# Performance work log

Measured on AMD Instinct MI355X. Metric: run time of the kernel, lower is better.

Reference implementation:

```python
import jax, jax.numpy as jnp
import numpy as np

# Fixed production-scale dims (equal-size graphs -> no ragged padding needed)
B, NPG, C, H, L, FFN, NC = 16, 512, 128, 8, 4, 512, 4
D = C // H          # head dim = 16
T = NPG + 1         # +1 virtual graph token
EPG = 8192          # edges per graph (avg degree 16)
E = B * EPG


def _ln(x, g, b, eps=1e-5):
    m = x.mean(-1, keepdims=True)
    v = ((x - m) ** 2).mean(-1, keepdims=True)
    return (x - m) * jax.lax.rsqrt(v + eps) * g + b


def setup_inputs() -> dict:
    key = jax.random.key(0)
    ks = jax.random.split(key, 24)
    N = B * NPG
    node_feats = jax.random.normal(ks[0], (N, 3), jnp.float32)
    # intra-graph edges: local endpoints + per-graph node offset (matches batch_ptr math)
    local = jax.random.randint(ks[1], (2, B, EPG), 0, NPG)
    offs = (jnp.arange(B) * NPG)[None, :, None]
    edge_index = (local + offs).reshape(2, E)
    edge_attr = jax.random.randint(ks[2], (E,), 0, 10)

    def nrm(k, shape, scale=0.02):
        return jax.random.normal(k, shape, jnp.float32) * scale

    params = {
        "W_node": nrm(ks[3], (3, C), 0.3), "b_node": jnp.zeros((C,), jnp.float32),
        "graph_token": nrm(ks[4], (C,), 1.0),
        "edge_bias_table": nrm(ks[5], (11, H), 0.1).at[0].set(0.0),  # padding_idx=0
        "in_deg_emb": nrm(ks[6], (512, C)).at[0].set(0.0),           # padding_idx=0
        "out_deg_emb": nrm(ks[7], (512, C)).at[0].set(0.0),
        "vnode_bias": nrm(ks[8], (H,), 1.0),
        "Wq": nrm(ks[9], (L, C, C)), "bq": jnp.zeros((L, C), jnp.float32),
        "Wk": nrm(ks[10], (L, C, C)), "bk": jnp.zeros((L, C), jnp.float32),
        "Wv": nrm(ks[11], (L, C, C)), "bv": jnp.zeros((L, C), jnp.float32),
        "Wo": nrm(ks[12], (L, C, C)), "bo": jnp.zeros((L, C), jnp.float32),
        "ln1_g": jnp.ones((L, C), jnp.float32), "ln1_b": jnp.zeros((L, C), jnp.float32),
        "ln2_g": jnp.ones((L, C), jnp.float32), "ln2_b": jnp.zeros((L, C), jnp.float32),
        "W1": nrm(ks[13], (L, C, FFN)), "b1": jnp.zeros((L, FFN), jnp.float32),
        "W2": nrm(ks[14], (L, FFN, C)), "b2": jnp.zeros((L, C), jnp.float32),
        "normf_g": jnp.ones((C,), jnp.float32), "normf_b": jnp.zeros((C,), jnp.float32),
        "Wc1": nrm(ks[15], (C, C // 2)), "bc1": jnp.zeros((C // 2,), jnp.float32),
        "Wc2": nrm(ks[16], (C // 2, NC)), "bc2": jnp.zeros((NC,), jnp.float32),
    }
    return {"node_feats": node_feats, "edge_index": edge_index,
            "edge_attr": edge_attr, "num_graphs": B, **params}


def reference(node_feats, W_node, b_node, graph_token, edge_bias_table,
              in_deg_emb, out_deg_emb, vnode_bias,
              Wq, bq, Wk, bk, Wv, bv, Wo, bo,
              ln1_g, ln1_b, ln2_g, ln2_b, W1, b1, W2, b2,
              normf_g, normf_b, Wc1, bc1, Wc2, bc2,
              edge_index, edge_attr, num_graphs):
    N = node_feats.shape[0]
    npg = N // num_graphs
    t = npg + 1
    src, dst = edge_index[0], edge_index[1]
    # degree encoders (scatter_add of ones == segment_sum)
    in_deg = jnp.clip(jax.ops.segment_sum(jnp.ones_like(dst), dst, num_segments=N), 0, 511)
    out_deg = jnp.clip(jax.ops.segment_sum(jnp.ones_like(src), src, num_segments=N), 0, 511)
    x_enc = node_feats @ W_node + b_node + in_deg_emb[in_deg] + out_deg_emb[out_deg]
    # equal-size graphs with sorted batch ids -> padding loop is a reshape, mask all-False
    x = jnp.concatenate(
        [jnp.broadcast_to(graph_token, (num_graphs, 1, C)),
         x_enc.reshape(num_graphs, npg, C)], axis=1)  # [B, T, C]
    # attention bias: vnode row/col + scattered edge-attr embeddings
    bias = jnp.zeros((num_graphs, H, t, t), jnp.float32)
    bias = bias.at[:, :, 0, :].set(vnode_bias[None, :, None])
    bias = bias.at[:, :, :, 0].set(vnode_bias[None, :, None])
    eb = edge_bias_table[jnp.clip(edge_attr, 0, 9) + 1]  # [E, H]
    g = src // npg
    sl = src - g * npg + 1
    dl = dst - g * npg + 1
    bias = bias.at[g, :, sl, dl].add(eb)  # duplicate edges accumulate (scatter_add)
    scale = 1.0 / np.sqrt(D).astype(np.float32)
    for l in range(L):  # key_padding_mask is all-False here -> masked_fill is a no-op
        h = _ln(x, ln1_g[l], ln1_b[l])
        q = (h @ Wq[l] + bq[l]).reshape(num_graphs, t, H, D)
        k = (h @ Wk[l] + bk[l]).reshape(num_graphs, t, H, D)
        v = (h @ Wv[l] + bv[l]).reshape(num_graphs, t, H, D)
        scores = jnp.einsum('bthd,bshd->bhts', q, k) * scale + bias
        attn = jax.nn.softmax(scores, axis=-1)
        o = jnp.einsum('bhts,bshd->bthd', attn, v).reshape(num_graphs, t, C)
        x = x + o @ Wo[l] + bo[l]
        h2 = _ln(x, ln2_g[l], ln2_b[l])
        x = x + jax.nn.gelu(h2 @ W1[l] + b1[l], approximate=False) @ W2[l] + b2[l]
    x = _ln(x, normf_g, normf_b)
    gr = x[:, 0, :]  # virtual-node readout
    return jax.nn.gelu(gr @ Wc1 + bc1, approximate=False) @ Wc2 + bc2
```

## Files before the change

kernel.cpp:

```cpp
#include <hip/hip_runtime.h>
#include <hip/hip_bf16.h>

#define BB 16
#define NPG 512
#define CC 128
#define HH 8
#define LL 4
#define FFN 512
#define NCLS 4
#define DD 16
#define TT 513
#define EE 131072
#define NNODES 8192
#define ROWS (BB * TT)
#define ECAP 64
#define SP 544
#define BSTR 292

static constexpr size_t XROWS = (size_t)BB * TT;
static constexpr size_t XSZ   = XROWS * CC;
static constexpr size_t VTSZ  = (size_t)BB * HH * DD * SP;

typedef unsigned short ushort_t;
typedef __attribute__((ext_vector_type(8))) short short8;
typedef __attribute__((ext_vector_type(4))) float floatx4;

__device__ __forceinline__ float gelu_exact(float v) {
    return 0.5f * v * (1.0f + erff(v * 0.70710678118654752440f));
}
__device__ __forceinline__ ushort_t f2bf(float f) {
    union { float f; unsigned u; } c; c.f = f;
    unsigned u = c.u;
    return (ushort_t)((u + 0x7FFFu + ((u >> 16) & 1u)) >> 16);
}
__device__ __forceinline__ int swz(int row, int col, int stride) {
    int kb = col >> 3;
    return row * stride + (((kb ^ (row & 7)) << 3) | (col & 7));
}

__device__ __forceinline__ void qkv_stage4(const ushort_t* hs,
                                           const ushort_t* Wtq, const float* bq_,
                                           const ushort_t* Wtk, const float* bk_,
                                           const ushort_t* Wtv, const float* bv_,
                                           ushort_t* qb, ushort_t* kb, ushort_t* vt,
                                           int b, int t0, int wave, int lq, int quad) {
    const short* hsS = (const short*)hs;
    int n0 = wave * 32;
    int c0 = n0 + lq, c1 = n0 + 16 + lq;
    const short* Ws[3] = {(const short*)Wtq, (const short*)Wtk, (const short*)Wtv};
    const float* bs[3] = {bq_, bk_, bv_};
    size_t rB0 = (size_t)(n0 + lq) * CC, rB1 = (size_t)(n0 + 16 + lq) * CC;

    #pragma unroll
    for (int m = 0; m < 3; ++m) {
        const short* W = Ws[m];
        floatx4 a0 = {0.f,0.f,0.f,0.f}, a1 = a0;
        #pragma unroll
        for (int k0 = 0; k0 < CC; k0 += 32) {
            short8 af = *(const short8*)(hsS + swz(lq, k0 + quad * 8, 128));
            short8 b0 = *(const short8*)(W + rB0 + k0 + quad * 8);
            short8 b1 = *(const short8*)(W + rB1 + k0 + quad * 8);
            a0 = __builtin_amdgcn_mfma_f32_16x16x32_bf16(af, b0, a0, 0, 0, 0);
            a1 = __builtin_amdgcn_mfma_f32_16x16x32_bf16(af, b1, a1, 0, 0, 0);
        }
        float bv0 = bs[m][c0], bv1 = bs[m][c1];
        #pragma unroll
        for (int rg = 0; rg < 4; ++rg) {
            int t = t0 + quad * 4 + rg;
            if (t >= TT) continue;
            size_t r = (size_t)b * TT + t;
            float v0 = a0[rg] + bv0;
            float v1 = a1[rg] + bv1;
            if (m == 0) {
                qb[r * CC + c0] = f2bf(v0 * 0.25f);
                qb[r * CC + c1] = f2bf(v1 * 0.25f);
            } else if (m == 1) {
                kb[r * CC + c0] = f2bf(v0);
                kb[r * CC + c1] = f2bf(v1);
            } else {
                vt[((size_t)(b * HH + (c0 >> 4)) * DD + (c0 & 15)) * SP + t] = f2bf(v0);
                vt[((size_t)(b * HH + (c1 >> 4)) * DD + (c1 & 15)) * SP + t] = f2bf(v1);
            }
        }
    }
}

__global__ __launch_bounds__(256) void deg_csr_tr_kernel(const int* __restrict__ ei,
                                                         const int* __restrict__ ea,
                                                         int* __restrict__ deg_in,
                                                         int* __restrict__ deg_out,
                                                         int* __restrict__ cnt,
                                                         int* __restrict__ ebuf,
                                                         const float* __restrict__ Wq,
                                                         const float* __restrict__ Wk,
                                                         const float* __restrict__ Wv,
                                                         const float* __restrict__ Wo,
                                                         const float* __restrict__ W1,
                                                         const float* __restrict__ W2,
                                                         ushort_t* __restrict__ wtqkvo,
                                                         ushort_t* __restrict__ wt1,
                                                         ushort_t* __restrict__ wt2) {
    int bid = blockIdx.x;
    int tid = threadIdx.x;
    if (bid < 512) {
        int e = bid * 256 + tid;
        int src = ei[e], dst = ei[EE + e];
        atomicAdd(&deg_out[src], 1);
        atomicAdd(&deg_in[dst], 1);
        int g = src >> 9;
        int sl = src - (g << 9) + 1;
        int dl = dst - (g << 9) + 1;
        int a = ea[e];
        a = (a < 0) ? 0 : (a > 9 ? 9 : a);
        a += 1;
        int row = g * TT + sl;
        int pos = atomicAdd(&cnt[row], 1);
        if (pos < ECAP) ebuf[(size_t)row * ECAP + pos] = dl | (a << 16);
        return;
    }
    int z = bid - 512;
    const float* src; ushort_t* dst; int K, N, tile;
    if (z < 64) {
        int zz = z >> 2; tile = z & 3;
        int k = zz >> 2, l = zz & 3;
        const float* s4[4] = {Wq, Wk, Wv, Wo};
        src = s4[k] + (size_t)l * CC * CC;
        dst = wtqkvo + (size_t)(k * 4 + l) * 16384;
        K = CC; N = CC;
    } else if (z < 128) {
        int l = (z - 64) >> 4; tile = (z - 64) & 15;
        src = W1 + (size_t)l * CC * FFN;
        dst = wt1 + (size_t)l * 65536;
        K = CC; N = FFN;
    } else {
        int l = (z - 128) >> 4; tile = (z - 128) & 15;
        src = W2 + (size_t)l * FFN * CC;
        dst = wt2 + (size_t)l * 65536;
        K = FFN; N = CC;
    }
    int tilesN = N >> 6;
    int k0 = (tile / tilesN) << 6;
    int n0 = (tile - (tile / tilesN) * tilesN) << 6;
    __shared__ float t[64][65];
    int c = tid & 63, rb = tid >> 6;
    #pragma unroll
    for (int kk = 0; kk < 64; kk += 4)
        t[kk + rb][c] = src[(size_t)(k0 + kk + rb) * N + n0 + c];
    __syncthreads();
    #pragma unroll
    for (int nn = 0; nn < 64; nn += 4)
        dst[(size_t)(n0 + nn + rb) * K + k0 + c] = f2bf(t[c][nn + rb]);
}

__global__ __launch_bounds__(256) void encode_pre_kernel(const float* __restrict__ nf,
                                                         const float* __restrict__ Wn,
                                                         const float* __restrict__ bn,
                                                         const float* __restrict__ gt,
                                                         const float* __restrict__ ide,
                                                         const float* __restrict__ ode,
                                                         const int* __restrict__ deg_in,
                                                         const int* __restrict__ deg_out,
                                                         const float* __restrict__ ln1g_,
                                                         const float* __restrict__ ln1b_,
                                                         const ushort_t* __restrict__ wtqkvo,
                                                         const float* __restrict__ bq_,
                                                         const float* __restrict__ bk_,
                                                         const float* __restrict__ bv_,
                                                         float* __restrict__ x_,
                                                         ushort_t* __restrict__ qb,
                                                         ushort_t* __restrict__ kb,
                                                         ushort_t* __restrict__ vt) {
    int qt = blockIdx.x, b = blockIdx.y;
    int t0 = qt * 16;
    int tid = threadIdx.x;
    int wave = tid >> 6, lane = tid & 63, lq = lane & 15, quad = lane >> 4;

    __shared__ ushort_t hs[16 * 128];
    __shared__ float sred[4][16][2];

    int n0 = wave * 32;
    int c0 = n0 + lq, c1 = n0 + 16 + lq;
    float w0[4], w1[4];
    #pragma unroll
    for (int rg = 0; rg < 4; ++rg) {
        int t = t0 + quad * 4 + rg;
        int tc = min(t, TT - 1);
        float v0, v1;
        if (tc == 0) {
            v0 = gt[c0]; v1 = gt[c1];
        } else {
            int i = b * NPG + tc - 1;
            float f0 = nf[i*3+0], f1 = nf[i*3+1], f2 = nf[i*3+2];
            v0 = bn[c0] + f0*Wn[0*CC + c0] + f1*Wn[1*CC + c0] + f2*Wn[2*CC + c0];
            v1 = bn[c1] + f0*Wn[0*CC + c1] + f1*Wn[1*CC + c1] + f2*Wn[2*CC + c1];
            int di = min(deg_in[i], 511);
            int dq = min(deg_out[i], 511);
            v0 += ide[(size_t)di * CC + c0] + ode[(size_t)dq * CC + c0];
            v1 += ide[(size_t)di * CC + c1] + ode[(size_t)dq * CC + c1];
        }
        if (t < TT) {
            size_t r = (size_t)b * TT + t;
            x_[r * CC + c0] = v0;
            x_[r * CC + c1] = v1;
        }
        w0[rg] = v0; w1[rg] = v1;
    }
    #pragma unroll
    for (int rg = 0; rg < 4; ++rg) {
        float s1 = w0[rg] + w1[rg];
        float s2 = w0[rg]*w0[rg] + w1[rg]*w1[rg];
        #pragma unroll
        for (int m = 1; m < 16; m <<= 1) {
            s1 += __shfl_xor(s1, m, 64);
            s2 += __shfl_xor(s2, m, 64);
        }
        if (lq == 0) { sred[wave][quad*4+rg][0] = s1; sred[wave][quad*4+rg][1] = s2; }
    }
    __syncthreads();
    float g0 = ln1g_[c0], g1 = ln1g_[c1], lb0 = ln1b_[c0], lb1 = ln1b_[c1];
    #pragma unroll
    for (int rg = 0; rg < 4; ++rg) {
        int row = quad * 4 + rg;
        float S1 = sred[0][row][0] + sred[1][row][0] + sred[2][row][0] + sred[3][row][0];
        float S2 = sred[0][row][1] + sred[1][row][1] + sred[2][row][1] + sred[3][row][1];
        float mn = S1 * (1.0f/CC);
        float var = S2 * (1.0f/CC) - mn * mn;
        float rs = rsqrtf(var + 1e-5f);
        hs[swz(row, c0, 128)] = f2bf((w0[rg] - mn) * rs * g0 + lb0);
        hs[swz(row, c1, 128)] = f2bf((w1[rg] - mn) * rs * g1 + lb1);
    }
    __syncthreads();
    qkv_stage4(hs, wtqkvo, bq_,
               wtqkvo + (size_t)4 * 16384, bk_,
               wtqkvo + (size_t)8 * 16384, bv_,
               qb, kb, vt, b, t0, wave, lq, quad);
}

__global__ __launch_bounds__(256) void layer_kernel(const ushort_t* __restrict__ qbr,
                                                    const ushort_t* __restrict__ kbr,
                                                    const ushort_t* __restrict__ vtr,
                                                    const int* __restrict__ cnt,
                                                    const int* __restrict__ ebuf,
                                                    const float* __restrict__ ebt,
                                                    const float* __restrict__ vnode,
                                                    const ushort_t* __restrict__ WtO,
                                                    const float* __restrict__ bo_,
                                                    const float* __restrict__ ln2g_,
                                                    const float* __restrict__ ln2b_,
                                                    const ushort_t* __restrict__ Wt1_,
                                                    const float* __restrict__ b1_,
                                                    const ushort_t* __restrict__ Wt2_,
                                                    const float* __restrict__ b2_,
                                                    const float* __restrict__ ln1g_,
                                                    const float* __restrict__ ln1b_,
                                                    const ushort_t* __restrict__ Wtq,
                                                    const float* __restrict__ bq_,
                                                    const ushort_t* __restrict__ Wtk,
                                                    const float* __restrict__ bk_,
                                                    const ushort_t* __restrict__ Wtv,
                                                    const float* __restrict__ bv_,
                                                    const float* __restrict__ nfg,
                                                    const float* __restrict__ nfb,
                                                    const float* __restrict__ Wc1,
                                                    const float* __restrict__ bc1,
                                                    const float* __restrict__ Wc2,
                                                    const float* __restrict__ bc2,
                                                    float* __restrict__ x_,
                                                    ushort_t* __restrict__ qbw,
                                                    ushort_t* __restrict__ kbw,
                                                    ushort_t* __restrict__ vtw,
                                                    float* __restrict__ out,
                                                    int doQKV) {
    int qt = blockIdx.x, b = blockIdx.y;
    int tid = threadIdx.x;
    int wave = tid >> 6, lane = tid & 63, lq = lane & 15, quad = lane >> 4;

    __shared__ __align__(16) char smem[20480];
    float* bstrip = (float*)smem;
    ushort_t* hs = (ushort_t*)smem;
    ushort_t* ms = (ushort_t*)(smem + 4096);
    __shared__ __align__(16) ushort_t obs[16 * 128];
    __shared__ float sred[4][16][2];

    int ql = tid >> 4, e0 = tid & 15;
    int qs = qt * 16 + ql;
    int crow = b * TT + (qs < TT ? qs : 0);
    int cn = (qs > 0 && qs < TT) ? min(cnt[crow], ECAP) : 0;
    int eh[4];
    #pragma unroll
    for (int jj = 0; jj < 4; ++jj) {
        int j = e0 + jj * 16;
        eh[jj] = (j < cn) ? ebuf[(size_t)crow * ECAP + j] : -1;
    }

    int qg = qt * 16 + lq;
    int qr = qg < TT ? qg : TT - 1;
    const short* kbS = (const short*)kbr;

    for (int h = 0; h < HH; ++h) {
        __syncthreads();
        short8 qf = {0,0,0,0,0,0,0,0};
        if (quad < 2)
            qf = *(const short8*)(qbr + ((size_t)(b * TT + qr)) * CC + h * DD + quad * 8);
        float vbh = vnode[h];
        const short* vtS = (const short*)(vtr + (size_t)(b * HH + h) * DD * SP);

        floatx4 oacc = {0.f, 0.f, 0.f, 0.f};
        float lsum = 0.f;

        #pragma unroll
        for (int ch = 0; ch < 2; ++ch) {
            int sp_lo = ch ? 9 : 0;
            int sp_hi = ch ? 17 : 9;
            int s_lo  = ch ? 288 : 0;
            int nrows = ch ? 256 : 288;

            int sp = sp_lo + wave;
            short8 af0 = {0,0,0,0,0,0,0,0}, af1 = af0, vf = af0;
            if (sp < sp_hi) {
                int st0 = sp * 2, st1 = sp * 2 + 1;
                int kr0 = min(b * TT + st0 * 16 + lq, (int)XROWS - 1);
                int kr1 = min(b * TT + st1 * 16 + lq, (int)XROWS - 1);
                if (quad < 2) {
                    af0 = *(const short8*)(kbS + (size_t)kr0 * CC + h * DD + quad * 8);
                    af1 = *(const short8*)(kbS + (size_t)kr1 * CC + h * DD + quad * 8);
                }
                vf = *(const short8*)(vtS + (size_t)lq * SP + sp * 32 + quad * 8);
            }

            for (int i = tid; i < 16 * BSTR / 4; i += 256)
                ((float4*)bstrip)[i] = make_float4(0.f, 0.f, 0.f, 0.f);
            __syncthreads();
            if (ch == 0 && tid < 16) {
                int q = qt * 16 + tid;
                if (q > 0 && q < TT) bstrip[tid * BSTR] = vbh;
            }
            #pragma unroll
            for (int jj = 0; jj < 4; ++jj) {
                int e = eh[jj];
                if (e >= 0) {
                    int dl = e & 0xFFFF, a = e >> 16;
                    int loc = dl - s_lo;
                    if (loc >= 0 && loc < nrows)
                        atomicAdd(&bstrip[ql * BSTR + loc], ebt[a * 8 + h]);
                }
            }
            __syncthreads();

            for (; sp < sp_hi; sp += 4) {
                int spn = sp + 4;
                short8 nf0 = {0,0,0,0,0,0,0,0}, nf1 = nf0, nvf = nf0;
                if (spn < sp_hi) {
                    int st0 = spn * 2, st1 = spn * 2 + 1;
                    int kr0 = min(b * TT + st0 * 16 + lq, (int)XROWS - 1);
                    int kr1 = min(b * TT + st1 * 16 + lq, (int)XROWS - 1);
                    if (quad < 2) {
                        nf0 = *(const short8*)(kbS + (size_t)kr0 * CC + h * DD + quad * 8);
                        nf1 = *(const short8*)(kbS + (size_t)kr1 * CC + h * DD + quad * 8);
                    }
                    nvf = *(const short8*)(vtS + (size_t)lq * SP + spn * 32 + quad * 8);
                }

                unsigned pw[2][2];
                #pragma unroll
                for (int t = 0; t < 2; ++t) {
                    int st = sp * 2 + t;
                    floatx4 c = __builtin_amdgcn_mfma_f32_16x16x32_bf16(
                        t ? af1 : af0, qf, (floatx4){0.f, 0.f, 0.f, 0.f}, 0, 0, 0);
                    float4 bi = *(const float4*)(bstrip + lq * BSTR + (st * 16 - s_lo) + quad * 4);
                    float biv[4] = {bi.x, bi.y, bi.z, bi.w};
                    float pr[4];
                    #pragma unroll
                    for (int rg = 0; rg < 4; ++rg) {
                        int s = st * 16 + quad * 4 + rg;
                        float p = 0.f;
                        if (s < TT) p = __expf(c[rg] + biv[rg]);
                        lsum += p;
                        pr[rg] = p;
                    }
                    pw[t][0] = (unsigned)f2bf(pr[0]) | ((unsigned)f2bf(pr[1]) << 16);
                    pw[t][1] = (unsigned)f2bf(pr[2]) | ((unsigned)f2bf(pr[3]) << 16);
                }
                int srcA = lq + (((2 * quad) & 3) << 4);
                int srcB = lq + (((2 * quad + 1) & 3) << 4);
                int a00 = __shfl((int)pw[0][0], srcA, 64);
                int a01 = __shfl((int)pw[0][1], srcA, 64);
                int a10 = __shfl((int)pw[1][0], srcA, 64);
                int a11 = __shfl((int)pw[1][1], srcA, 64);
                int b00 = __shfl((int)pw[0][0], srcB, 64);
                int b01 = __shfl((int)pw[0][1], srcB, 64);
                int b10 = __shfl((int)pw[1][0], srcB, 64);
                int b11 = __shfl((int)pw[1][1], srcB, 64);
                union { int u[4]; short8 s8; } pu;
                bool lo = quad < 2;
                pu.u[0] = lo ? a00 : a10;
                pu.u[1] = lo ? a01 : a11;
                pu.u[2] = lo ? b00 : b10;
                pu.u[3] = lo ? b01 : b11;
                oacc = __builtin_amdgcn_mfma_f32_16x16x32_bf16(vf, pu.s8, oacc, 0, 0, 0);

                af0 = nf0; af1 = nf1; vf = nvf;
            }
            __syncthreads();
        }

        lsum += __shfl_xor(lsum, 16, 64);
        lsum += __shfl_xor(lsum, 32, 64);
        float* redw = (float*)smem;
        float* lsumS = (float*)smem + 1088;
        #pragma unroll
        for (int rg = 0; rg < 4; ++rg)
            redw[wave * 272 + (quad * 4 + rg) * 17 + lq] = oacc[rg];
        if (quad == 0) lsumS[wave * 16 + lq] = lsum;
        __syncthreads();
        {
            int q = tid >> 4, d = tid & 15;
            float o = 0.f, L = 0.f;
            #pragma unroll
            for (int w = 0; w < 4; ++w) {
                o += redw[w * 272 + d * 17 + q];
                L += lsumS[w * 16 + q];
            }
            obs[swz(q, h * DD + d, 128)] = f2bf(o / L);
        }
    }
    __syncthreads();

    int t0 = qt * 16;
    int n0 = wave * 32;
    int c0 = n0 + lq, c1 = n0 + 16 + lq;
    float vv0[4], vv1[4];
    const short* obsS = (const short*)obs;

    {
        const short* W = (const short*)WtO;
        size_t rB0 = (size_t)(n0 + lq) * CC, rB1 = (size_t)(n0 + 16 + lq) * CC;
        floatx4 a0 = {0.f,0.f,0.f,0.f}, a1 = a0;
        #pragma unroll
        for (int k0 = 0; k0 < CC; k0 += 32) {
            short8 af = *(const short8*)(obsS + swz(lq, k0 + quad * 8, 128));
            short8 b0 = *(const short8*)(W + rB0 + k0 + quad * 8);
            short8 b1 = *(const short8*)(W + rB1 + k0 + quad * 8);
            a0 = __builtin_amdgcn_mfma_f32_16x16x32_bf16(af, b0, a0, 0, 0, 0);
            a1 = __builtin_amdgcn_mfma_f32_16x16x32_bf16(af, b1, a1, 0, 0, 0);
        }
        float bv0 = bo_[c0], bv1 = bo_[c1];
        #pragma unroll
        for (int rg = 0; rg < 4; ++rg) {
            int t = t0 + quad * 4 + rg;
            size_t rc = (size_t)b * TT + min(t, TT - 1);
            vv0[rg] = a0[rg] + bv0 + x_[rc * CC + c0];
            vv1[rg] = a1[rg] + bv1 + x_[rc * CC + c1];
        }
        #pragma unroll
        for (int rg = 0; rg < 4; ++rg) {
            float s1 = vv0[rg] + vv1[rg];
            float s2 = vv0[rg]*vv0[rg] + vv1[rg]*vv1[rg];
            #pragma unroll
            for (int m = 1; m < 16; m <<= 1) {
                s1 += __shfl_xor(s1, m, 64);
                s2 += __shfl_xor(s2, m, 64);
            }
            if (lq == 0) { sred[wave][quad*4+rg][0] = s1; sred[wave][quad*4+rg][1] = s2; }
        }
        __syncthreads();
        float g0 = ln2g_[c0], g1 = ln2g_[c1], lb0 = ln2b_[c0], lb1 = ln2b_[c1];
        #pragma unroll
        for (int rg = 0; rg < 4; ++rg) {
            int row = quad * 4 + rg;
            float S1 = sred[0][row][0] + sred[1][row][0] + sred[2][row][0] + sred[3][row][0];
            float S2 = sred[0][row][1] + sred[1][row][1] + sred[2][row][1] + sred[3][row][1];
            float mn = S1 * (1.0f/CC);
            float var = S2 * (1.0f/CC) - mn * mn;
            float rs = rsqrtf(var + 1e-5f);
            hs[swz(row, c0, 128)] = f2bf((vv0[rg] - mn) * rs * g0 + lb0);
            hs[swz(row, c1, 128)] = f2bf((vv1[rg] - mn) * rs * g1 + lb1);
        }
    }
    __syncthreads();

    {
        const short* hsS = (const short*)hs;
        const short* W = (const short*)Wt1_;
        #pragma unroll
        for (int nt = 0; nt < 4; ++nt) {
            int n = wave * 128 + nt * 32;
            size_t rB0 = (size_t)(n + lq) * CC, rB1 = (size_t)(n + 16 + lq) * CC;
            floatx4 a0 = {0.f,0.f,0.f,0.f}, a1 = a0;
            #pragma unroll
            for (int k0 = 0; k0 < CC; k0 += 32) {
                short8 af = *(const short8*)(hsS + swz(lq, k0 + quad * 8, 128));
                short8 b0 = *(const short8*)(W + rB0 + k0 + quad * 8);
                short8 b1 = *(const short8*)(W + rB1 + k0 + quad * 8);
                a0 = __builtin_amdgcn_mfma_f32_16x16x32_bf16(af, b0, a0, 0, 0, 0);
                a1 = __builtin_amdgcn_mfma_f32_16x16x32_bf16(af, b1, a1, 0, 0, 0);
            }
            float bb0 = b1_[n + lq], bb1 = b1_[n + 16 + lq];
            #pragma unroll
            for (int rg = 0; rg < 4; ++rg) {
                int row = quad * 4 + rg;
                ms[swz(row, n + lq, 512)]      = f2bf(gelu_exact(a0[rg] + bb0));
                ms[swz(row, n + 16 + lq, 512)] = f2bf(gelu_exact(a1[rg] + bb1));
            }
        }
    }
    __syncthreads();

    float w0[4], w1[4];
    {
        const short* msS = (const short*)ms;
        const short* W = (const short*)Wt2_;
        size_t rB0 = (size_t)(n0 + lq) * FFN, rB1 = (size_t)(n0 + 16 + lq) * FFN;
        floatx4 a0 = {0.f,0.f,0.f,0.f}, a1 = a0;
        #pragma unroll 8
        for (int k0 = 0; k0 < FFN; k0 += 32) {
            short8 af = *(const short8*)(msS + swz(lq, k0 + quad * 8, 512));
            short8 b0 = *(const short8*)(W + rB0 + k0 + quad * 8);
            short8 b1 = *(const short8*)(W + rB1 + k0 + quad * 8);
            a0 = __builtin_amdgcn_mfma_f32_16x16x32_bf16(af, b0, a0, 0, 0, 0);
            a1 = __builtin_amdgcn_mfma_f32_16x16x32_bf16(af, b1, a1, 0, 0, 0);
        }
        float bv0 = b2_[c0], bv1 = b2_[c1];
        #pragma unroll
        for (int rg = 0; rg < 4; ++rg) {
            int t = t0 + quad * 4 + rg;
            w0[rg] = a0[rg] + bv0 + vv0[rg];
            w1[rg] = a1[rg] + bv1 + vv1[rg];
            if (t < TT) {
                size_t r = (size_t)b * TT + t;
                x_[r * CC + c0] = w0[rg];
                x_[r * CC + c1] = w1[rg];
            }
        }
    }

    if (doQKV) {
        #pragma unroll
        for (int rg = 0; rg < 4; ++rg) {
            float s1 = w0[rg] + w1[rg];
            float s2 = w0[rg]*w0[rg] + w1[rg]*w1[rg];
            #pragma unroll
            for (int m = 1; m < 16; m <<= 1) {
                s1 += __shfl_xor(s1, m, 64);
                s2 += __shfl_xor(s2, m, 64);
            }
            if (lq == 0) { sred[wave][quad*4+rg][0] = s1; sred[wave][quad*4+rg][1] = s2; }
        }
        __syncthreads();
        float g0 = ln1g_[c0], g1 = ln1g_[c1], lb0 = ln1b_[c0], lb1 = ln1b_[c1];
        #pragma unroll
        for (int rg = 0; rg < 4; ++rg) {
            int row = quad * 4 + rg;
            float S1 = sred[0][row][0] + sred[1][row][0] + sred[2][row][0] + sred[3][row][0];
            float S2 = sred[0][row][1] + sred[1][row][1] + sred[2][row][1] + sred[3][row][1];
            float mn = S1 * (1.0f/CC);
            float var = S2 * (1.0f/CC) - mn * mn;
            float rs = rsqrtf(var + 1e-5f);
            hs[swz(row, c0, 128)] = f2bf((w0[rg] - mn) * rs * g0 + lb0);
            hs[swz(row, c1, 128)] = f2bf((w1[rg] - mn) * rs * g1 + lb1);
        }
        __syncthreads();
        qkv_stage4(hs, Wtq, bq_, Wtk, bk_, Wtv, bv_, qbw, kbw, vtw, b, t0, wave, lq, quad);
        return;
    }

    if (qt != 0) return;

    __syncthreads();
    float* hrow = (float*)ms;
    float* xfs  = hrow + CC;
    float* c1s  = xfs + CC;
    float* red  = c1s + 64;
    #pragma unroll
    for (int rg = 0; rg < 4; ++rg) {
        if (quad * 4 + rg == 0) { hrow[c0] = w0[rg]; hrow[c1] = w1[rg]; }
    }
    __syncthreads();

    {
        int c = tid;
        float v = 0.f, s1 = 0.f, s2 = 0.f;
        if (c < CC) { v = hrow[c]; s1 = v; s2 = v * v; }
        #pragma unroll
        for (int m = 32; m >= 1; m >>= 1) {
            s1 += __shfl_xor(s1, m, 64);
            s2 += __shfl_xor(s2, m, 64);
        }
        int w = c >> 6;
        if (c < CC && (c & 63) == 0) { red[w*2] = s1; red[w*2+1] = s2; }
        __syncthreads();
        if (c < CC) {
            float S1 = red[0] + red[2], S2 = red[1] + red[3];
            float mn = S1 * (1.0f/CC);
            float var = S2 * (1.0f/CC) - mn * mn;
            float rs = rsqrtf(var + 1e-5f);
            xfs[c] = (v - mn) * rs * nfg[c] + nfb[c];
        }
        __syncthreads();
        if (c < 64) {
            float acc = bc1[c];
            #pragma unroll 4
            for (int k = 0; k < CC; ++k) acc = fmaf(xfs[k], Wc1[(size_t)k * 64 + c], acc);
            c1s[c] = gelu_exact(acc);
        }
        __syncthreads();
        if (c < NCLS) {
            float acc = bc2[c];
            #pragma unroll 4
            for (int j = 0; j < 64; ++j) acc = fmaf(c1s[j], Wc2[(size_t)j * NCLS + c], acc);
            out[(size_t)b * NCLS + c] = acc;
        }
    }
}

extern "C" void kernel_launch(void* const* d_in, const int* in_sizes, int n_in,
                              void* d_out, int out_size, void* d_ws, size_t ws_size,
                              hipStream_t stream) {
    const float* node_feats = (const float*)d_in[0];
    const int*   edge_index = (const int*)d_in[1];
    const int*   edge_attr  = (const int*)d_in[2];
    const float* W_node  = (const float*)d_in[4];
    const float* b_node  = (const float*)d_in[5];
    const float* g_token = (const float*)d_in[6];
    const float* ebt     = (const float*)d_in[7];
    const float* ide     = (const float*)d_in[8];
    const float* ode     = (const float*)d_in[9];
    const float* vnode   = (const float*)d_in[10];
    const float* Wq = (const float*)d_in[11];
    const float* bq = (const float*)d_in[12];
    const float* Wk = (const float*)d_in[13];
    const float* bk = (const float*)d_in[14];
    const float* Wv = (const float*)d_in[15];
    const float* bv = (const float*)d_in[16];
    const float* Wo = (const float*)d_in[17];
    const float* bo = (const float*)d_in[18];
    const float* ln1g = (const float*)d_in[19];
    const float* ln1b = (const float*)d_in[20];
    const float* ln2g = (const float*)d_in[21];
    const float* ln2b = (const float*)d_in[22];
    const float* W1 = (const float*)d_in[23];
    const float* b1 = (const float*)d_in[24];
    const float* W2 = (const float*)d_in[25];
    const float* b2 = (const float*)d_in[26];
    const float* nfg = (const float*)d_in[27];
    const float* nfb = (const float*)d_in[28];
    const float* Wc1 = (const float*)d_in[29];
    const float* bc1 = (const float*)d_in[30];
    const float* Wc2 = (const float*)d_in[31];
    const float* bc2 = (const float*)d_in[32];
    float* out = (float*)d_out;

    char* base = (char*)d_ws;
    float* x      = (float*)base;     base += XSZ * 4;
    ushort_t* qb0 = (ushort_t*)base;  base += XSZ * 2;
    ushort_t* kb0 = (ushort_t*)base;  base += XSZ * 2;
    ushort_t* vt0 = (ushort_t*)base;  base += VTSZ * 2;
    ushort_t* qb1 = (ushort_t*)base;  base += XSZ * 2;
    ushort_t* kb1 = (ushort_t*)base;  base += XSZ * 2;
    ushort_t* vt1 = (ushort_t*)base;  base += VTSZ * 2;
    ushort_t* wtqkvo = (ushort_t*)base; base += (size_t)16 * 16384 * 2;
    ushort_t* wt1 = (ushort_t*)base;  base += (size_t)4 * 65536 * 2;
    ushort_t* wt2 = (ushort_t*)base;  base += (size_t)4 * 65536 * 2;
    int* deg_in  = (int*)base;        base += NNODES * 4;
    int* deg_out = (int*)base;        base += NNODES * 4;
    int* cnt     = (int*)base;        base += (size_t)ROWS * 4;
    int* ebuf    = (int*)base;        base += (size_t)ROWS * ECAP * 4;

    ushort_t* qbs[2] = {qb0, qb1};
    ushort_t* kbs[2] = {kb0, kb1};
    ushort_t* vts[2] = {vt0, vt1};

    hipMemsetAsync(deg_in, 0, (size_t)(2 * NNODES + ROWS) * 4, stream);
    deg_csr_tr_kernel<<<512 + 192, 256, 0, stream>>>(
        edge_index, edge_attr, deg_in, deg_out, cnt, ebuf,
        Wq, Wk, Wv, Wo, W1, W2, wtqkvo, wt1, wt2);

    encode_pre_kernel<<<dim3(33, BB), 256, 0, stream>>>(
        node_feats, W_node, b_node, g_token, ide, ode, deg_in, deg_out,
        ln1g, ln1b, wtqkvo, bq, bk, bv, x, qb0, kb0, vt0);

    for (int l = 0; l < LL; ++l) {
        int rd = l & 1, wr = rd ^ 1;
        int ln = (l + 1) % LL;
        layer_kernel<<<dim3(33, BB), 256, 0, stream>>>(
            qbs[rd], kbs[rd], vts[rd], cnt, ebuf, ebt, vnode,
            wtqkvo + (size_t)(12 + l)*16384, bo + l*CC,
            ln2g + l*CC, ln2b + l*CC,
            wt1 + (size_t)l*65536, b1 + l*FFN,
            wt2 + (size_t)l*65536, b2 + l*CC,
            ln1g + ln*CC, ln1b + ln*CC,
            wtqkvo + (size_t)(0 + ln)*16384, bq + ln*CC,
            wtqkvo + (size_t)(4 + ln)*16384, bk + ln*CC,
            wtqkvo + (size_t)(8 + ln)*16384, bv + ln*CC,
            nfg, nfb, Wc1, bc1, Wc2, bc2,
            x, qbs[wr], kbs[wr], vts[wr], out,
            (l < LL-1) ? 1 : 0);
    }
}
```

Baseline: 474.2 us.

## Precompute dense bf16 edge-bias tensor once and widen blocks to 512 threads

Adds a pre-pass, run inside the same pre_kernel launch, that builds a dense bf16 attention-bias tensor [B,H,513,544] from the per-row edge lists. Each layer then reads this tensor instead of rebuilding the sparse bias from cnt/ebuf four times. Separately, every kernel moves from 4 to 8 waves per block, with each wave handling 16 output columns instead of 32, to raise parallelism. The cost is a roughly 36 MB extra bias buffer that must be streamed from memory in every layer, plus more synchronisation per block.

```diff
diff --git a/kernel.cpp b/kernel.cpp
--- a/kernel.cpp
+++ b/kernel.cpp
@@ -15,11 +15,12 @@
 #define ROWS (BB * TT)
 #define ECAP 64
 #define SP 544
-#define BSTR 292
+#define BPAD 544
 
 static constexpr size_t XROWS = (size_t)BB * TT;
 static constexpr size_t XSZ   = XROWS * CC;
 static constexpr size_t VTSZ  = (size_t)BB * HH * DD * SP;
+static constexpr size_t BIASSZ = (size_t)BB * HH * 513 * BPAD;
 
 typedef unsigned short ushort_t;
 typedef __attribute__((ext_vector_type(8))) short short8;
@@ -33,53 +34,49 @@
     unsigned u = c.u;
     return (ushort_t)((u + 0x7FFFu + ((u >> 16) & 1u)) >> 16);
 }
+__device__ __forceinline__ float bf2f(ushort_t u) {
+    union { unsigned u; float f; } c; c.u = ((unsigned)u) << 16; return c.f;
+}
 __device__ __forceinline__ int swz(int row, int col, int stride) {
     int kb = col >> 3;
     return row * stride + (((kb ^ (row & 7)) << 3) | (col & 7));
 }
 
-__device__ __forceinline__ void qkv_stage4(const ushort_t* hs,
+__device__ __forceinline__ void qkv_stage8(const ushort_t* hs,
                                            const ushort_t* Wtq, const float* bq_,
                                            const ushort_t* Wtk, const float* bk_,
                                            const ushort_t* Wtv, const float* bv_,
                                            ushort_t* qb, ushort_t* kb, ushort_t* vt,
                                            int b, int t0, int wave, int lq, int quad) {
     const short* hsS = (const short*)hs;
-    int n0 = wave * 32;
-    int c0 = n0 + lq, c1 = n0 + 16 + lq;
+    int c = wave * 16 + lq;
     const short* Ws[3] = {(const short*)Wtq, (const short*)Wtk, (const short*)Wtv};
     const float* bs[3] = {bq_, bk_, bv_};
-    size_t rB0 = (size_t)(n0 + lq) * CC, rB1 = (size_t)(n0 + 16 + lq) * CC;
+    size_t rB = (size_t)c * CC;
 
     #pragma unroll
     for (int m = 0; m < 3; ++m) {
         const short* W = Ws[m];
-        floatx4 a0 = {0.f,0.f,0.f,0.f}, a1 = a0;
+        floatx4 a0 = {0.f,0.f,0.f,0.f};
         #pragma unroll
         for (int k0 = 0; k0 < CC; k0 += 32) {
             short8 af = *(const short8*)(hsS + swz(lq, k0 + quad * 8, 128));
-            short8 b0 = *(const short8*)(W + rB0 + k0 + quad * 8);
-            short8 b1 = *(const short8*)(W + rB1 + k0 + quad * 8);
+            short8 b0 = *(const short8*)(W + rB + k0 + quad * 8);
             a0 = __builtin_amdgcn_mfma_f32_16x16x32_bf16(af, b0, a0, 0, 0, 0);
-            a1 = __builtin_amdgcn_mfma_f32_16x16x32_bf16(af, b1, a1, 0, 0, 0);
-        }
-        float bv0 = bs[m][c0], bv1 = bs[m][c1];
+        }
+        float bv0 = bs[m][c];
         #pragma unroll
         for (int rg = 0; rg < 4; ++rg) {
             int t = t0 + quad * 4 + rg;
             if (t >= TT) continue;
             size_t r = (size_t)b * TT + t;
             float v0 = a0[rg] + bv0;
-            float v1 = a1[rg] + bv1;
             if (m == 0) {
-                qb[r * CC + c0] = f2bf(v0 * 0.25f);
-                qb[r * CC + c1] = f2bf(v1 * 0.25f);
+                qb[r * CC + c] = f2bf(v0 * 0.25f);
             } else if (m == 1) {
-                kb[r * CC + c0] = f2bf(v0);
-                kb[r * CC + c1] = f2bf(v1);
+                kb[r * CC + c] = f2bf(v0);
             } else {
-                vt[((size_t)(b * HH + (c0 >> 4)) * DD + (c0 & 15)) * SP + t] = f2bf(v0);
-                vt[((size_t)(b * HH + (c1 >> 4)) * DD + (c1 & 15)) * SP + t] = f2bf(v1);
+                vt[((size_t)(b * HH + wave) * DD + lq) * SP + t] = f2bf(v0);
             }
         }
     }
@@ -152,63 +149,87 @@
         dst[(size_t)(n0 + nn + rb) * K + k0 + c] = f2bf(t[c][nn + rb]);
 }
 
-__global__ __launch_bounds__(256) void encode_pre_kernel(const float* __restrict__ nf,
-                                                         const float* __restrict__ Wn,
-                                                         const float* __restrict__ bn,
-                                                         const float* __restrict__ gt,
-                                                         const float* __restrict__ ide,
-                                                         const float* __restrict__ ode,
-                                                         const int* __restrict__ deg_in,
-                                                         const int* __restrict__ deg_out,
-                                                         const float* __restrict__ ln1g_,
-                                                         const float* __restrict__ ln1b_,
-                                                         const ushort_t* __restrict__ wtqkvo,
-                                                         const float* __restrict__ bq_,
-                                                         const float* __restrict__ bk_,
-                                                         const float* __restrict__ bv_,
-                                                         float* __restrict__ x_,
-                                                         ushort_t* __restrict__ qb,
-                                                         ushort_t* __restrict__ kb,
-                                                         ushort_t* __restrict__ vt) {
-    int qt = blockIdx.x, b = blockIdx.y;
+__global__ __launch_bounds__(512) void pre_kernel(const float* __restrict__ nf,
+                                                  const float* __restrict__ Wn,
+                                                  const float* __restrict__ bn,
+                                                  const float* __restrict__ gt,
+                                                  const float* __restrict__ ide,
+                                                  const float* __restrict__ ode,
+                                                  const int* __restrict__ deg_in,
+                                                  const int* __restrict__ deg_out,
+                                                  const float* __restrict__ ln1g_,
+                                                  const float* __restrict__ ln1b_,
+                                                  const ushort_t* __restrict__ wtqkvo,
+                                                  const float* __restrict__ bq_,
+                                                  const float* __restrict__ bk_,
+                                                  const float* __restrict__ bv_,
+                                                  float* __restrict__ x_,
+                                                  ushort_t* __restrict__ qb,
+                                                  ushort_t* __restrict__ kb,
+                                                  ushort_t* __restrict__ vt,
+                                                  const int* __restrict__ cnt,
+                                                  const int* __restrict__ ebuf,
+                                                  const float* __restrict__ ebt,
+                                                  ushort_t* __restrict__ bias_d) {
+    int bid = blockIdx.x;
+    int tid = threadIdx.x;
+    __shared__ __align__(16) char parena[17408];
+
+    if (bid >= 528) {
+        int z = bid - 528;
+        int b = z / 513;
+        int sl = z - b * 513;
+        float* row8 = (float*)parena;
+        for (int i = tid; i < 8 * BPAD / 4; i += 512)
+            ((float4*)row8)[i] = make_float4(0.f, 0.f, 0.f, 0.f);
+        __syncthreads();
+        int crow = b * TT + sl;
+        int cn = min(cnt[crow], ECAP);
+        int h = tid & 7;
+        for (int j = tid >> 3; j < cn; j += 64) {
+            int e = ebuf[(size_t)crow * ECAP + j];
+            atomicAdd(&row8[h * BPAD + (e & 0xFFFF)], ebt[(e >> 16) * 8 + h]);
+        }
+        __syncthreads();
+        #pragma unroll
+        for (int hh = 0; hh < HH; ++hh) {
+            size_t base = ((size_t)(b * HH + hh) * 513 + sl) * BPAD;
+            for (int s = tid; s < BPAD; s += 512)
+                bias_d[base + s] = f2bf(row8[hh * BPAD + s]);
+        }
+        return;
+    }
+
+    int b = bid / 33, qt = bid - b * 33;
     int t0 = qt * 16;
-    int tid = threadIdx.x;
     int wave = tid >> 6, lane = tid & 63, lq = lane & 15, quad = lane >> 4;
-
-    __shared__ ushort_t hs[16 * 128];
-    __shared__ float sred[4][16][2];
-
-    int n0 = wave * 32;
-    int c0 = n0 + lq, c1 = n0 + 16 + lq;
-    float w0[4], w1[4];
+    ushort_t* hs = (ushort_t*)parena;
+    auto sred = (float (*)[16][2])(parena + 4096);
+
+    int c = wave * 16 + lq;
+    float w0[4];
     #pragma unroll
     for (int rg = 0; rg < 4; ++rg) {
         int t = t0 + quad * 4 + rg;
         int tc = min(t, TT - 1);
-        float v0, v1;
+        float v0;
         if (tc == 0) {
-            v0 = gt[c0]; v1 = gt[c1];
+            v0 = gt[c];
         } else {
             int i = b * NPG + tc - 1;
             float f0 = nf[i*3+0], f1 = nf[i*3+1], f2 = nf[i*3+2];
-            v0 = bn[c0] + f0*Wn[0*CC + c0] + f1*Wn[1*CC + c0] + f2*Wn[2*CC + c0];
-            v1 = bn[c1] + f0*Wn[0*CC + c1] + f1*Wn[1*CC + c1] + f2*Wn[2*CC + c1];
+            v0 = bn[c] + f0*Wn[0*CC + c] + f1*Wn[1*CC + c] + f2*Wn[2*CC + c];
             int di = min(deg_in[i], 511);
             int dq = min(deg_out[i], 511);
-            v0 += ide[(size_t)di * CC + c0] + ode[(size_t)dq * CC + c0];
-            v1 += ide[(size_t)di * CC + c1] + ode[(size_t)dq * CC + c1];
-        }
-        if (t < TT) {
-            size_t r = (size_t)b * TT + t;
-            x_[r * CC + c0] = v0;
-            x_[r * CC + c1] = v1;
-        }
-        w0[rg] = v0; w1[rg] = v1;
+            v0 += ide[(size_t)di * CC + c] + ode[(size_t)dq * CC + c];
+        }
+        if (t < TT) x_[((size_t)b * TT + t) * CC + c] = v0;
+        w0[rg] = v0;
     }
     #pragma unroll
     for (int rg = 0; rg < 4; ++rg) {
-        float s1 = w0[rg] + w1[rg];
-        float s2 = w0[rg]*w0[rg] + w1[rg]*w1[rg];
+        float s1 = w0[rg];
+        float s2 = w0[rg] * w0[rg];
         #pragma unroll
         for (int m = 1; m < 16; m <<= 1) {
             s1 += __shfl_xor(s1, m, 64);
@@ -217,245 +238,192 @@
         if (lq == 0) { sred[wave][quad*4+rg][0] = s1; sred[wave][quad*4+rg][1] = s2; }
     }
     __syncthreads();
-    float g0 = ln1g_[c0], g1 = ln1g_[c1], lb0 = ln1b_[c0], lb1 = ln1b_[c1];
+    float g0 = ln1g_[c], lb0 = ln1b_[c];
     #pragma unroll
     for (int rg = 0; rg < 4; ++rg) {
         int row = quad * 4 + rg;
-        float S1 = sred[0][row][0] + sred[1][row][0] + sred[2][row][0] + sred[3][row][0];
-        float S2 = sred[0][row][1] + sred[1][row][1] + sred[2][row][1] + sred[3][row][1];
+        float S1 = 0.f, S2 = 0.f;
+        #pragma unroll
+        for (int w = 0; w < 8; ++w) { S1 += sred[w][row][0]; S2 += sred[w][row][1]; }
         float mn = S1 * (1.0f/CC);
         float var = S2 * (1.0f/CC) - mn * mn;
         float rs = rsqrtf(var + 1e-5f);
-        hs[swz(row, c0, 128)] = f2bf((w0[rg] - mn) * rs * g0 + lb0);
-        hs[swz(row, c1, 128)] = f2bf((w1[rg] - mn) * rs * g1 + lb1);
-    }
-    __syncthreads();
-    qkv_stage4(hs, wtqkvo, bq_,
+        hs[swz(row, c, 128)] = f2bf((w0[rg] - mn) * rs * g0 + lb0);
+    }
+    __syncthreads();
+    qkv_stage8(hs, wtqkvo, bq_,
                wtqkvo + (size_t)4 * 16384, bk_,
                wtqkvo + (size_t)8 * 16384, bv_,
                qb, kb, vt, b, t0, wave, lq, quad);
 }
 
-__global__ __launch_bounds__(256) void layer_kernel(const ushort_t* __restrict__ qbr,
-                                                    const ushort_t* __restrict__ kbr,
-                                                    const ushort_t* __restrict__ vtr,
-                                                    const int* __restrict__ cnt,
-                                                    const int* __restrict__ ebuf,
-                                                    const float* __restrict__ ebt,
-                                                    const float* __restrict__ vnode,
-                                                    const ushort_t* __restrict__ WtO,
-                                                    const float* __restrict__ bo_,
-                                                    const float* __restrict__ ln2g_,
-                                                    const float* __restrict__ ln2b_,
-                                                    const ushort_t* __restrict__ Wt1_,
-                                                    const float* __restrict__ b1_,
-                                                    const ushort_t* __restrict__ Wt2_,
-                                                    const float* __restrict__ b2_,
-                                                    const float* __restrict__ ln1g_,
-                                                    const float* __restrict__ ln1b_,
-                                                    const ushort_t* __restrict__ Wtq,
-                                                    const float* __restrict__ bq_,
-                                                    const ushort_t* __restrict__ Wtk,
-                                                    const float* __restrict__ bk_,
-                                                    const ushort_t* __restrict__ Wtv,
-                                                    const float* __restrict__ bv_,
-                                                    const float* __restrict__ nfg,
-                                                    const float* __restrict__ nfb,
-                                                    const float* __restrict__ Wc1,
-                                                    const float* __restrict__ bc1,
-                                                    const float* __restrict__ Wc2,
-                                                    const float* __restrict__ bc2,
-                                                    float* __restrict__ x_,
-                                                    ushort_t* __restrict__ qbw,
-                                                    ushort_t* __restrict__ kbw,
-                                                    ushort_t* __restrict__ vtw,
-                                                    float* __restrict__ out,
-                                                    int doQKV) {
+__global__ __launch_bounds__(512, 4) void layer_kernel(const ushort_t* __restrict__ qbr,
+                                                       const ushort_t* __restrict__ kbr,
+                                                       const ushort_t* __restrict__ vtr,
+                                                       const ushort_t* __restrict__ bias_d,
+                                                       const float* __restrict__ vnode,
+                                                       const ushort_t* __restrict__ WtO,
+                                                       const float* __restrict__ bo_,
+                                                       const float* __restrict__ ln2g_,
+                                                       const float* __restrict__ ln2b_,
+                                                       const ushort_t* __restrict__ Wt1_,
+                                                       const float* __restrict__ b1_,
+                                                       const ushort_t* __restrict__ Wt2_,
+                                                       const float* __restrict__ b2_,
+                                                       const float* __restrict__ ln1g_,
+                                                       const float* __restrict__ ln1b_,
+                                                       const ushort_t* __restrict__ Wtq,
+                                                       const float* __restrict__ bq_,
+                                                       const ushort_t* __restrict__ Wtk,
+                                                       const float* __restrict__ bk_,
+                                                       const ushort_t* __restrict__ Wtv,
+                                                       const float* __restrict__ bv_,
+                                                       const float* __restrict__ nfg,
+                                                       const float* __restrict__ nfb,
+                                                       const float* __restrict__ Wc1,
+                                                       const float* __restrict__ bc1,
+                                                       const float* __restrict__ Wc2,
+                                                       const float* __restrict__ bc2,
+                                                       float* __restrict__ x_,
+                                                       ushort_t* __restrict__ qbw,
+                                                       ushort_t* __restrict__ kbw,
+                                                       ushort_t* __restrict__ vtw,
+                                                       float* __restrict__ out,
+                                                       int doQKV) {
     int qt = blockIdx.x, b = blockIdx.y;
     int tid = threadIdx.x;
     int wave = tid >> 6, lane = tid & 63, lq = lane & 15, quad = lane >> 4;
 
     __shared__ __align__(16) char smem[20480];
-    float* bstrip = (float*)smem;
     ushort_t* hs = (ushort_t*)smem;
     ushort_t* ms = (ushort_t*)(smem + 4096);
     __shared__ __align__(16) ushort_t obs[16 * 128];
-    __shared__ float sred[4][16][2];
-
-    int ql = tid >> 4, e0 = tid & 15;
-    int qs = qt * 16 + ql;
-    int crow = b * TT + (qs < TT ? qs : 0);
-    int cn = (qs > 0 && qs < TT) ? min(cnt[crow], ECAP) : 0;
-    int eh[4];
-    #pragma unroll
-    for (int jj = 0; jj < 4; ++jj) {
-        int j = e0 + jj * 16;
-        eh[jj] = (j < cn) ? ebuf[(size_t)crow * ECAP + j] : -1;
-    }
-
-    int qg = qt * 16 + lq;
-    int qr = qg < TT ? qg : TT - 1;
-    const short* kbS = (const short*)kbr;
-
-    for (int h = 0; h < HH; ++h) {
-        __syncthreads();
-        short8 qf = {0,0,0,0,0,0,0,0};
+    __shared__ float sred[8][16][2];
+
+    {
+        int h = wave;
+        int qg = qt * 16 + lq;
+        int qr = min(qg, TT - 1);
+        short8 z8 = {0,0,0,0,0,0,0,0};
+        short8 qf = z8;
         if (quad < 2)
             qf = *(const short8*)(qbr + ((size_t)(b * TT + qr)) * CC + h * DD + quad * 8);
-        float vbh = vnode[h];
+        float vn = vnode[h];
+        const short* kbS = (const short*)kbr;
         const short* vtS = (const short*)(vtr + (size_t)(b * HH + h) * DD * SP);
+        const ushort_t* brow = bias_d + ((size_t)(b * HH + h) * 513 + qr) * BPAD;
+
+        short8 af0c = z8, af1c = z8, vfc;
+        {
+            int kr0 = min(b * TT + lq, (int)XROWS - 1);
+            int kr1 = min(b * TT + 16 + lq, (int)XROWS - 1);
+            if (quad < 2) {
+                af0c = *(const short8*)(kbS + (size_t)kr0 * CC + h * DD + quad * 8);
+                af1c = *(const short8*)(kbS + (size_t)kr1 * CC + h * DD + quad * 8);
+            }
+            vfc = *(const short8*)(vtS + (size_t)lq * SP + quad * 8);
+        }
+        uint2 bi0c = *(const uint2*)(brow + quad * 4);
+        uint2 bi1c = *(const uint2*)(brow + 16 + quad * 4);
 
         floatx4 oacc = {0.f, 0.f, 0.f, 0.f};
         float lsum = 0.f;
 
-        #pragma unroll
-        for (int ch = 0; ch < 2; ++ch) {
-            int sp_lo = ch ? 9 : 0;
-            int sp_hi = ch ? 17 : 9;
-            int s_lo  = ch ? 288 : 0;
-            int nrows = ch ? 256 : 288;
-
-            int sp = sp_lo + wave;
-            short8 af0 = {0,0,0,0,0,0,0,0}, af1 = af0, vf = af0;
-            if (sp < sp_hi) {
-                int st0 = sp * 2, st1 = sp * 2 + 1;
+        for (int sp = 0; sp < 17; ++sp) {
+            int spn = sp + 1;
+            short8 af0n = z8, af1n = z8, vfn = z8;
+            uint2 bi0n = make_uint2(0u, 0u), bi1n = make_uint2(0u, 0u);
+            if (spn < 17) {
+                int st0 = spn * 2, st1 = st0 + 1;
                 int kr0 = min(b * TT + st0 * 16 + lq, (int)XROWS - 1);
                 int kr1 = min(b * TT + st1 * 16 + lq, (int)XROWS - 1);
                 if (quad < 2) {
-                    af0 = *(const short8*)(kbS + (size_t)kr0 * CC + h * DD + quad * 8);
-                    af1 = *(const short8*)(kbS + (size_t)kr1 * CC + h * DD + quad * 8);
+                    af0n = *(const short8*)(kbS + (size_t)kr0 * CC + h * DD + quad * 8);
+                    af1n = *(const short8*)(kbS + (size_t)kr1 * CC + h * DD + quad * 8);
                 }
-                vf = *(const short8*)(vtS + (size_t)lq * SP + sp * 32 + quad * 8);
+                vfn = *(const short8*)(vtS + (size_t)lq * SP + spn * 32 + quad * 8);
+                bi0n = *(const uint2*)(brow + spn * 32 + quad * 4);
+                bi1n = *(const uint2*)(brow + spn * 32 + 16 + quad * 4);
             }
-
-            for (int i = tid; i < 16 * BSTR / 4; i += 256)
-                ((float4*)bstrip)[i] = make_float4(0.f, 0.f, 0.f, 0.f);
-            __syncthreads();
-            if (ch == 0 && tid < 16) {
-                int q = qt * 16 + tid;
-                if (q > 0 && q < TT) bstrip[tid * BSTR] = vbh;
+            float vadd = ((sp == 0) & (quad == 0) & (qg > 0)) ? vn : 0.f;
+
+            unsigned pw[2][2];
+            #pragma unroll
+            for (int t = 0; t < 2; ++t) {
+                int st = sp * 2 + t;
+                floatx4 cc4 = __builtin_amdgcn_mfma_f32_16x16x32_bf16(
+                    t ? af1c : af0c, qf, (floatx4){0.f, 0.f, 0.f, 0.f}, 0, 0, 0);
+                uint2 bi = t ? bi1c : bi0c;
+                float pr[4];
+                #pragma unroll
+                for (int rg = 0; rg < 4; ++rg) {
+                    int s = st * 16 + quad * 4 + rg;
+                    unsigned bw = (rg < 2) ? bi.x : bi.y;
+                    float bb = bf2f((rg & 1) ? (ushort_t)(bw >> 16) : (ushort_t)(bw & 0xFFFFu));
+                    if (t == 0 && rg == 0) bb += vadd;
+                    float p = 0.f;
+                    if (s < TT) p = __expf(cc4[rg] + bb);
+                    lsum += p;
+                    pr[rg] = p;
+                }
+                pw[t][0] = (unsigned)f2bf(pr[0]) | ((unsigned)f2bf(pr[1]) << 16);
+                pw[t][1] = (unsigned)f2bf(pr[2]) | ((unsigned)f2bf(pr[3]) << 16);
             }
-            #pragma unroll
-            for (int jj = 0; jj < 4; ++jj) {
-                int e = eh[jj];
-                if (e >= 0) {
-                    int dl = e & 0xFFFF, a = e >> 16;
-                    int loc = dl - s_lo;
-                    if (loc >= 0 && loc < nrows)
-                        atomicAdd(&bstrip[ql * BSTR + loc], ebt[a * 8 + h]);
-                }
-            }
-            __syncthreads();
-
-            for (; sp < sp_hi; sp += 4) {
-                int spn = sp + 4;
-                short8 nf0 = {0,0,0,0,0,0,0,0}, nf1 = nf0, nvf = nf0;
-                if (spn < sp_hi) {
-                    int st0 = spn * 2, st1 = spn * 2 + 1;
-                    int kr0 = min(b * TT + st0 * 16 + lq, (int)XROWS - 1);
-                    int kr1 = min(b * TT + st1 * 16 + lq, (int)XROWS - 1);
-                    if (quad < 2) {
-                        nf0 = *(const short8*)(kbS + (size_t)kr0 * CC + h * DD + quad * 8);
-                        nf1 = *(const short8*)(kbS + (size_t)kr1 * CC + h * DD + quad * 8);
-                    }
-                    nvf = *(const short8*)(vtS + (size_t)lq * SP + spn * 32 + quad * 8);
-                }
-
-                unsigned pw[2][2];
-                #pragma unroll
-                for (int t = 0; t < 2; ++t) {
-                    int st = sp * 2 + t;
-                    floatx4 c = __builtin_amdgcn_mfma_f32_16x16x32_bf16(
-                        t ? af1 : af0, qf, (floatx4){0.f, 0.f, 0.f, 0.f}, 0, 0, 0);
-                    float4 bi = *(const float4*)(bstrip + lq * BSTR + (st * 16 - s_lo) + quad * 4);
-                    float biv[4] = {bi.x, bi.y, bi.z, bi.w};
-                    float pr[4];
-                    #pragma unroll
-                    for (int rg = 0; rg < 4; ++rg) {
-                        int s = st * 16 + quad * 4 + rg;
-                        float p = 0.f;
-                        if (s < TT) p = __expf(c[rg] + biv[rg]);
-                        lsum += p;
-                        pr[rg] = p;
-                    }
-                    pw[t][0] = (unsigned)f2bf(pr[0]) | ((unsigned)f2bf(pr[1]) << 16);
-                    pw[t][1] = (unsigned)f2bf(pr[2]) | ((unsigned)f2bf(pr[3]) << 16);
-                }
-                int srcA = lq + (((2 * quad) & 3) << 4);
-                int srcB = lq + (((2 * quad + 1) & 3) << 4);
-                int a00 = __shfl((int)pw[0][0], srcA, 64);
-                int a01 = __shfl((int)pw[0][1], srcA, 64);
-                int a10 = __shfl((int)pw[1][0], srcA, 64);
-                int a11 = __shfl((int)pw[1][1], srcA, 64);
-                int b00 = __shfl((int)pw[0][0], srcB, 64);
-                int b01 = __shfl((int)pw[0][1], srcB, 64);
-                int b10 = __shfl((int)pw[1][0], srcB, 64);
-                int b11 = __shfl((int)pw[1][1], srcB, 64);
-                union { int u[4]; short8 s8; } pu;
-                bool lo = quad < 2;
-                pu.u[0] = lo ? a00 : a10;
-                pu.u[1] = lo ? a01 : a11;
-                pu.u[2] = lo ? b00 : b10;
-                pu.u[3] = lo ? b01 : b11;
-                oacc = __builtin_amdgcn_mfma_f32_16x16x32_bf16(vf, pu.s8, oacc, 0, 0, 0);
-
-                af0 = nf0; af1 = nf1; vf = nvf;
-            }
-            __syncthreads();
+            int srcA = lq + (((2 * quad) & 3) << 4);
+            int srcB = lq + (((2 * quad + 1) & 3) << 4);
+            int a00 = __shfl((int)pw[0][0], srcA, 64);
+            int a01 = __shfl((int)pw[0][1], srcA, 64);
+            int a10 = __shfl((int)pw[1][0], srcA, 64);
+            int a11 = __shfl((int)pw[1][1], srcA, 64);
+            int b00 = __shfl((int)pw[0][0], srcB, 64);
+            int b01 = __shfl((int)pw[0][1], srcB, 64);
+            int b10 = __shfl((int)pw[1][0], srcB, 64);
+            int b11 = __shfl((int)pw[1][1], srcB, 64);
+            union { int u[4]; short8 s8; } pu;
+            bool lo = quad < 2;
+            pu.u[0] = lo ? a00 : a10;
+            pu.u[1] = lo ? a01 : a11;
+            pu.u[2] = lo ? b00 : b10;
+            pu.u[3] = lo ? b01 : b11;
+            oacc = __builtin_amdgcn_mfma_f32_16x16x32_bf16(vfc, pu.s8, oacc, 0, 0, 0);
+
+            af0c = af0n; af1c = af1n; vfc = vfn; bi0c = bi0n; bi1c = bi1n;
         }
 
         lsum += __shfl_xor(lsum, 16, 64);
         lsum += __shfl_xor(lsum, 32, 64);
-        float* redw = (float*)smem;
-        float* lsumS = (float*)smem + 1088;
         #pragma unroll
         for (int rg = 0; rg < 4; ++rg)
-            redw[wave * 272 + (quad * 4 + rg) * 17 + lq] = oacc[rg];
-        if (quad == 0) lsumS[wave * 16 + lq] = lsum;
-        __syncthreads();
-        {
-            int q = tid >> 4, d = tid & 15;
-            float o = 0.f, L = 0.f;
-            #pragma unroll
-            for (int w = 0; w < 4; ++w) {
-                o += redw[w * 272 + d * 17 + q];
-                L += lsumS[w * 16 + q];
-            }
-            obs[swz(q, h * DD + d, 128)] = f2bf(o / L);
-        }
+            obs[swz(lq, h * DD + quad * 4 + rg, 128)] = f2bf(oacc[rg] / lsum);
     }
     __syncthreads();
 
     int t0 = qt * 16;
-    int n0 = wave * 32;
-    int c0 = n0 + lq, c1 = n0 + 16 + lq;
-    float vv0[4], vv1[4];
+    int c = wave * 16 + lq;
+    float vv0[4];
     const short* obsS = (const short*)obs;
 
     {
         const short* W = (const short*)WtO;
-        size_t rB0 = (size_t)(n0 + lq) * CC, rB1 = (size_t)(n0 + 16 + lq) * CC;
-        floatx4 a0 = {0.f,0.f,0.f,0.f}, a1 = a0;
+        size_t rB = (size_t)c * CC;
+        floatx4 a0 = {0.f,0.f,0.f,0.f};
         #pragma unroll
         for (int k0 = 0; k0 < CC; k0 += 32) {
             short8 af = *(const short8*)(obsS + swz(lq, k0 + quad * 8, 128));
-            short8 b0 = *(const short8*)(W + rB0 + k0 + quad * 8);
-            short8 b1 = *(const short8*)(W + rB1 + k0 + quad * 8);
+            short8 b0 = *(const short8*)(W + rB + k0 + quad * 8);
             a0 = __builtin_amdgcn_mfma_f32_16x16x32_bf16(af, b0, a0, 0, 0, 0);
-            a1 = __builtin_amdgcn_mfma_f32_16x16x32_bf16(af, b1, a1, 0, 0, 0);
-        }
-        float bv0 = bo_[c0], bv1 = bo_[c1];
+        }
+        float bv0 = bo_[c];
         #pragma unroll
         for (int rg = 0; rg < 4; ++rg) {
             int t = t0 + quad * 4 + rg;
             size_t rc = (size_t)b * TT + min(t, TT - 1);
-            vv0[rg] = a0[rg] + bv0 + x_[rc * CC + c0];
-            vv1[rg] = a1[rg] + bv1 + x_[rc * CC + c1];
+            vv0[rg] = a0[rg] + bv0 + x_[rc * CC + c];
         }
         #pragma unroll
         for (int rg = 0; rg < 4; ++rg) {
-            float s1 = vv0[rg] + vv1[rg];
-            float s2 = vv0[rg]*vv0[rg] + vv1[rg]*vv1[rg];
+            float s1 = vv0[rg];
+            float s2 = vv0[rg] * vv0[rg];
             #pragma unroll
             for (int m = 1; m < 16; m <<= 1) {
                 s1 += __shfl_xor(s1, m, 64);
@@ -464,17 +432,17 @@
             if (lq == 0) { sred[wave][quad*4+rg][0] = s1; sred[wave][quad*4+rg][1] = s2; }
         }
         __syncthreads();
-        float g0 = ln2g_[c0], g1 = ln2g_[c1], lb0 = ln2b_[c0], lb1 = ln2b_[c1];
+        float g0 = ln2g_[c], lb0 = ln2b_[c];
         #pragma unroll
         for (int rg = 0; rg < 4; ++rg) {
             int row = quad * 4 + rg;
-            float S1 = sred[0][row][0] + sred[1][row][0] + sred[2][row][0] + sred[3][row][0];
-            float S2 = sred[0][row][1] + sred[1][row][1] + sred[2][row][1] + sred[3][row][1];
+            float S1 = 0.f, S2 = 0.f;
+            #pragma unroll
+            for (int w = 0; w < 8; ++w) { S1 += sred[w][row][0]; S2 += sred[w][row][1]; }
             float mn = S1 * (1.0f/CC);
             float var = S2 * (1.0f/CC) - mn * mn;
             float rs = rsqrtf(var + 1e-5f);
-            hs[swz(row, c0, 128)] = f2bf((vv0[rg] - mn) * rs * g0 + lb0);
-            hs[swz(row, c1, 128)] = f2bf((vv1[rg] - mn) * rs * g1 + lb1);
+            hs[swz(row, c, 128)] = f2bf((vv0[rg] - mn) * rs * g0 + lb0);
         }
     }
     __syncthreads();
@@ -484,61 +452,49 @@
         const short* W = (const short*)Wt1_;
         #pragma unroll
         for (int nt = 0; nt < 4; ++nt) {
-            int n = wave * 128 + nt * 32;
-            size_t rB0 = (size_t)(n + lq) * CC, rB1 = (size_t)(n + 16 + lq) * CC;
-            floatx4 a0 = {0.f,0.f,0.f,0.f}, a1 = a0;
+            int n = wave * 64 + nt * 16;
+            size_t rB = (size_t)(n + lq) * CC;
+            floatx4 a0 = {0.f,0.f,0.f,0.f};
             #pragma unroll
             for (int k0 = 0; k0 < CC; k0 += 32) {
                 short8 af = *(const short8*)(hsS + swz(lq, k0 + quad * 8, 128));
-                short8 b0 = *(const short8*)(W + rB0 + k0 + quad * 8);
-                short8 b1 = *(const short8*)(W + rB1 + k0 + quad * 8);
+                short8 b0 = *(const short8*)(W + rB + k0 + quad * 8);
                 a0 = __builtin_amdgcn_mfma_f32_16x16x32_bf16(af, b0, a0, 0, 0, 0);
-                a1 = __builtin_amdgcn_mfma_f32_16x16x32_bf16(af, b1, a1, 0, 0, 0);
             }
-            float bb0 = b1_[n + lq], bb1 = b1_[n + 16 + lq];
+            float bb0 = b1_[n + lq];
             #pragma unroll
-            for (int rg = 0; rg < 4; ++rg) {
-                int row = quad * 4 + rg;
-                ms[swz(row, n + lq, 512)]      = f2bf(gelu_exact(a0[rg] + bb0));
-                ms[swz(row, n + 16 + lq, 512)] = f2bf(gelu_exact(a1[rg] + bb1));
-            }
-        }
-    }
-    __syncthreads();
-
-    float w0[4], w1[4];
+            for (int rg = 0; rg < 4; ++rg)
+                ms[swz(quad * 4 + rg, n + lq, 512)] = f2bf(gelu_exact(a0[rg] + bb0));
+        }
+    }
+    __syncthreads();
+
+    float w0[4];
     {
         const short* msS = (const short*)ms;
         const short* W = (const short*)Wt2_;
-        size_t rB0 = (size_t)(n0 + lq) * FFN, rB1 = (size_t)(n0 + 16 + lq) * FFN;
-        floatx4 a0 = {0.f,0.f,0.f,0.f}, a1 = a0;
+        size_t rB = (size_t)c * FFN;
+        floatx4 a0 = {0.f,0.f,0.f,0.f};
         #pragma unroll 8
         for (int k0 = 0; k0 < FFN; k0 += 32) {
             short8 af = *(const short8*)(msS + swz(lq, k0 + quad * 8, 512));
-            short8 b0 = *(const short8*)(W + rB0 + k0 + quad * 8);
-            short8 b1 = *(const short8*)(W + rB1 + k0 + quad * 8);
+            short8 b0 = *(const short8*)(W + rB + k0 + quad * 8);
             a0 = __builtin_amdgcn_mfma_f32_16x16x32_bf16(af, b0, a0, 0, 0, 0);
-            a1 = __builtin_amdgcn_mfma_f32_16x16x32_bf16(af, b1, a1, 0, 0, 0);
-        }
-        float bv0 = b2_[c0], bv1 = b2_[c1];
+        }
+        float bv0 = b2_[c];
         #pragma unroll
         for (int rg = 0; rg < 4; ++rg) {
             int t = t0 + quad * 4 + rg;
             w0[rg] = a0[rg] + bv0 + vv0[rg];
-            w1[rg] = a1[rg] + bv1 + vv1[rg];
-            if (t < TT) {
-                size_t r = (size_t)b * TT + t;
-                x_[r * CC + c0] = w0[rg];
-                x_[r * CC + c1] = w1[rg];
-            }
+            if (t < TT) x_[((size_t)b * TT + t) * CC + c] = w0[rg];
         }
     }
 
     if (doQKV) {
         #pragma unroll
         for (int rg = 0; rg < 4; ++rg) {
-            float s1 = w0[rg] + w1[rg];
-            float s2 = w0[rg]*w0[rg] + w1[rg]*w1[rg];
+            float s1 = w0[rg];
+            float s2 = w0[rg] * w0[rg];
             #pragma unroll
             for (int m = 1; m < 16; m <<= 1) {
                 s1 += __shfl_xor(s1, m, 64);
@@ -547,20 +503,20 @@
             if (lq == 0) { sred[wave][quad*4+rg][0] = s1; sred[wave][quad*4+rg][1] = s2; }
         }
         __syncthreads();
-        float g0 = ln1g_[c0], g1 = ln1g_[c1], lb0 = ln1b_[c0], lb1 = ln1b_[c1];
+        float g0 = ln1g_[c], lb0 = ln1b_[c];
         #pragma unroll
         for (int rg = 0; rg < 4; ++rg) {
             int row = quad * 4 + rg;
-            float S1 = sred[0][row][0] + sred[1][row][0] + sred[2][row][0] + sred[3][row][0];
-            float S2 = sred[0][row][1] + sred[1][row][1] + sred[2][row][1] + sred[3][row][1];
+            float S1 = 0.f, S2 = 0.f;
+            #pragma unroll
+            for (int w = 0; w < 8; ++w) { S1 += sred[w][row][0]; S2 += sred[w][row][1]; }
             float mn = S1 * (1.0f/CC);
             float var = S2 * (1.0f/CC) - mn * mn;
             float rs = rsqrtf(var + 1e-5f);
-            hs[swz(row, c0, 128)] = f2bf((w0[rg] - mn) * rs * g0 + lb0);
-            hs[swz(row, c1, 128)] = f2bf((w1[rg] - mn) * rs * g1 + lb1);
-        }
-        __syncthreads();
-        qkv_stage4(hs, Wtq, bq_, Wtk, bk_, Wtv, bv_, qbw, kbw, vtw, b, t0, wave, lq, quad);
+            hs[swz(row, c, 128)] = f2bf((w0[rg] - mn) * rs * g0 + lb0);
+        }
+        __syncthreads();
+        qkv_stage8(hs, Wtq, bq_, Wtk, bk_, Wtv, bv_, qbw, kbw, vtw, b, t0, wave, lq, quad);
         return;
     }
 
@@ -571,44 +527,41 @@
     float* xfs  = hrow + CC;
     float* c1s  = xfs + CC;
     float* red  = c1s + 64;
-    #pragma unroll
-    for (int rg = 0; rg < 4; ++rg) {
-        if (quad * 4 + rg == 0) { hrow[c0] = w0[rg]; hrow[c1] = w1[rg]; }
-    }
+    if (quad == 0) hrow[c] = w0[0];
     __syncthreads();
 
     {
-        int c = tid;
+        int ct = tid;
         float v = 0.f, s1 = 0.f, s2 = 0.f;
-        if (c < CC) { v = hrow[c]; s1 = v; s2 = v * v; }
+        if (ct < CC) { v = hrow[ct]; s1 = v; s2 = v * v; }
         #pragma unroll
         for (int m = 32; m >= 1; m >>= 1) {
             s1 += __shfl_xor(s1, m, 64);
             s2 += __shfl_xor(s2, m, 64);
         }
-        int w = c >> 6;
-        if (c < CC && (c & 63) == 0) { red[w*2] = s1; red[w*2+1] = s2; }
-        __syncthreads();
-        if (c < CC) {
+        int w = ct >> 6;
+        if (ct < CC && (ct & 63) == 0) { red[w*2] = s1; red[w*2+1] = s2; }
+        __syncthreads();
+        if (ct < CC) {
             float S1 = red[0] + red[2], S2 = red[1] + red[3];
             float mn = S1 * (1.0f/CC);
             float var = S2 * (1.0f/CC) - mn * mn;
             float rs = rsqrtf(var + 1e-5f);
-            xfs[c] = (v - mn) * rs * nfg[c] + nfb[c];
-        }
-        __syncthreads();
-        if (c < 64) {
-            float acc = bc1[c];
+            xfs[ct] = (v - mn) * rs * nfg[ct] + nfb[ct];
+        }
+        __syncthreads();
+        if (ct < 64) {
+            float acc = bc1[ct];
             #pragma unroll 4
-            for (int k = 0; k < CC; ++k) acc = fmaf(xfs[k], Wc1[(size_t)k * 64 + c], acc);
-            c1s[c] = gelu_exact(acc);
-        }
-        __syncthreads();
-        if (c < NCLS) {
-            float acc = bc2[c];
+            for (int k = 0; k < CC; ++k) acc = fmaf(xfs[k], Wc1[(size_t)k * 64 + ct], acc);
+            c1s[ct] = gelu_exact(acc);
+        }
+        __syncthreads();
+        if (ct < NCLS) {
+            float acc = bc2[ct];
             #pragma unroll 4
-            for (int j = 0; j < 64; ++j) acc = fmaf(c1s[j], Wc2[(size_t)j * NCLS + c], acc);
-            out[(size_t)b * NCLS + c] = acc;
+            for (int j = 0; j < 64; ++j) acc = fmaf(c1s[j], Wc2[(size_t)j * NCLS + ct], acc);
+            out[(size_t)b * NCLS + ct] = acc;
         }
     }
 }
@@ -661,6 +614,7 @@
     ushort_t* wtqkvo = (ushort_t*)base; base += (size_t)16 * 16384 * 2;
     ushort_t* wt1 = (ushort_t*)base;  base += (size_t)4 * 65536 * 2;
     ushort_t* wt2 = (ushort_t*)base;  base += (size_t)4 * 65536 * 2;
+    ushort_t* bias_d = (ushort_t*)base; base += BIASSZ * 2;
     int* deg_in  = (int*)base;        base += NNODES * 4;
     int* deg_out = (int*)base;        base += NNODES * 4;
     int* cnt     = (int*)base;        base += (size_t)ROWS * 4;
@@ -675,15 +629,16 @@
         edge_index, edge_attr, deg_in, deg_out, cnt, ebuf,
         Wq, Wk, Wv, Wo, W1, W2, wtqkvo, wt1, wt2);
 
-    encode_pre_kernel<<<dim3(33, BB), 256, 0, stream>>>(
+    pre_kernel<<<528 + 8208, 512, 0, stream>>>(
         node_feats, W_node, b_node, g_token, ide, ode, deg_in, deg_out,
-        ln1g, ln1b, wtqkvo, bq, bk, bv, x, qb0, kb0, vt0);
+        ln1g, ln1b, wtqkvo, bq, bk, bv, x, qb0, kb0, vt0,
+        cnt, ebuf, ebt, bias_d);
 
     for (int l = 0; l < LL; ++l) {
         int rd = l & 1, wr = rd ^ 1;
         int ln = (l + 1) % LL;
-        layer_kernel<<<dim3(33, BB), 256, 0, stream>>>(
-            qbs[rd], kbs[rd], vts[rd], cnt, ebuf, ebt, vnode,
+        layer_kernel<<<dim3(33, BB), 512, 0, stream>>>(
+            qbs[rd], kbs[rd], vts[rd], bias_d, vnode,
             wtqkvo + (size_t)(12 + l)*16384, bo + l*CC,
             ln2g + l*CC, ln2b + l*CC,
             wt1 + (size_t)l*65536, b1 + l*FFN,
```

Result: faster. 464.8 us (-2.0%).
